# Optimization experiments

Hardware: AMD Instinct MI355X
Metric: run time of the kernel (lower is better)

Reference implementation:

```python
import jax, jax.numpy as jnp
import numpy as np
from jax import lax

B, T, I, H = 64, 784, 1, 600


def setup_inputs() -> dict:
    key = jax.random.key(0)
    ks = jax.random.split(key, 9)
    k = 1.0 / np.sqrt(H)  # pytorch LSTMCell/Linear init scale
    x = jax.random.normal(ks[0], (B, T, I), dtype=jnp.float32)
    hs0 = jax.random.normal(ks[1], (B, H), dtype=jnp.float32)
    cs0 = jax.random.normal(ks[2], (B, H), dtype=jnp.float32)
    W_ih = jax.random.normal(ks[3], (4 * H, I), dtype=jnp.float32) * k
    W_hh = jax.random.normal(ks[4], (4 * H, H), dtype=jnp.float32) * k
    b_ih = jax.random.normal(ks[5], (4 * H,), dtype=jnp.float32) * k
    b_hh = jax.random.normal(ks[6], (4 * H,), dtype=jnp.float32) * k
    W_out = jax.random.normal(ks[7], (10, H), dtype=jnp.float32) * k
    b_out = jax.random.normal(ks[8], (10,), dtype=jnp.float32) * k
    return {"x": x, "hs0": hs0, "cs0": cs0, "W_ih": W_ih, "W_hh": W_hh,
            "b_ih": b_ih, "b_hh": b_hh, "W_out": W_out, "b_out": b_out}


def reference(x, hs0, cs0, W_ih, W_hh, b_ih, b_hh, W_out, b_out):
    # Precompute input projections for all timesteps in one GEMM: [B,T,4H]
    pre = jnp.einsum('bti,gi->btg', x, W_ih) + b_ih + b_hh
    pre_t = jnp.swapaxes(pre, 0, 1)  # [T,B,4H]

    def step(carry, p):
        h, c = carry
        gates = p + h @ W_hh.T  # [B,4H], pytorch gate order i,f,g,o
        i, f, g, o = jnp.split(gates, 4, axis=-1)
        c = jax.nn.sigmoid(f) * c + jax.nn.sigmoid(i) * jnp.tanh(g)
        h = jax.nn.sigmoid(o) * jnp.tanh(c)
        return (h, c), None

    (h, _), _ = lax.scan(step, (hs0, cs0), pre_t)
    return h @ W_out.T + b_out  # [B,10]
```

## Files before the change

### kernel.cpp

```cpp
#include <hip/hip_runtime.h>
#include <math.h>

#define BB 64
#define TT 784
#define HH 600
#define CG 50
#define SGN 4
#define CPW 12
#define BW 16
#define NWG (CG*SGN)
#define BLOCK 512
#define HB4 (BW*150)
#define LDS_BYTES (84*1024)

__device__ __forceinline__ float dot4acc(float4 a, float4 b, float acc) {
    acc = fmaf(a.x, b.x, acc);
    acc = fmaf(a.y, b.y, acc);
    acc = fmaf(a.z, b.z, acc);
    acc = fmaf(a.w, b.w, acc);
    return acc;
}

__device__ __forceinline__ void ldg5_bypass(const float4* g0, const float4* g1,
                                            const float4* g2, const float4* g3,
                                            const float4* g4,
                                            float4& a, float4& b, float4& c,
                                            float4& d, float4& e) {
    asm volatile(
        "global_load_dwordx4 %0, %5, off sc0 sc1\n\t"
        "global_load_dwordx4 %1, %6, off sc0 sc1\n\t"
        "global_load_dwordx4 %2, %7, off sc0 sc1\n\t"
        "global_load_dwordx4 %3, %8, off sc0 sc1\n\t"
        "global_load_dwordx4 %4, %9, off sc0 sc1\n\t"
        "s_waitcnt vmcnt(0)"
        : "=&v"(a), "=&v"(b), "=&v"(c), "=&v"(d), "=&v"(e)
        : "v"(g0), "v"(g1), "v"(g2), "v"(g3), "v"(g4)
        : "memory");
}

__device__ __forceinline__ void stg_bypass(float* p, float v) {
    asm volatile("global_store_dword %0, %1, off sc0 sc1"
                 :: "v"(p), "v"(v) : "memory");
}

__device__ __forceinline__ float sigm_f(float v) {
    return 1.f / (1.f + __expf(-v));
}
__device__ __forceinline__ float tanh_f(float v) {
    return 1.f - 2.f / (__expf(2.f * v) + 1.f);
}

template<int MASK, int CNT>
__device__ __forceinline__ void fold(float* v, int kh) {
    const bool hi = (kh & MASK) != 0;
    #pragma unroll
    for (int i = 0; i < CNT; ++i) {
        float send = hi ? v[i] : v[i + CNT];
        float recv = __shfl_xor(send, MASK);
        v[i] = (hi ? v[i + CNT] : v[i]) + recv;
    }
}

extern "C" __global__ void __launch_bounds__(BLOCK, 2)
lstm_main(const float* __restrict__ x, const float* __restrict__ hs0,
          const float* __restrict__ cs0, const float* __restrict__ W_ih,
          const float* __restrict__ W_hh, const float* __restrict__ b_ih,
          const float* __restrict__ b_hh, float* __restrict__ hbuf,
          unsigned int* __restrict__ flags)
{
    extern __shared__ float lds[];
    float4* h4l  = (float4*)lds;
    float*  g_lds = lds + 4 * HB4;

    const int wg   = blockIdx.x;
    const int cg   = wg % CG;
    const int sg   = wg / CG;
    const int tid  = threadIdx.x;
    const int w    = tid >> 6;
    const int lane = tid & 63;
    const int bh   = lane >> 5;
    const int kh   = lane & 31;
    const int khc  = (kh < 30) ? kh : 29;
    const int b0   = sg * BW;

    float4 Wr[6][5];
    #pragma unroll
    for (int r = 0; r < 6; ++r) {
        const int row = 6 * w + r;
        const int g   = row / 12, c = row % 12;
        const float* wrow = W_hh + ((size_t)g * HH + cg * CPW + c) * HH + khc * 20;
        #pragma unroll
        for (int j = 0; j < 5; ++j)
            Wr[r][j] = (kh < 30) ? *(const float4*)(wrow + 4 * j)
                                 : make_float4(0.f, 0.f, 0.f, 0.f);
    }

    float wihv[4], biasv[4], cst = 0.f;
    const int pc = tid >> 4, pb = tid & 15;
    const int cell = cg * CPW + pc;
    const int bglob = b0 + pb;
    if (tid < 192) {
        #pragma unroll
        for (int g = 0; g < 4; ++g) {
            const int grow = g * HH + cell;
            wihv[g]  = W_ih[grow];
            biasv[g] = b_ih[grow] + b_hh[grow];
        }
        cst = cs0[(size_t)bglob * HH + cell];
    }

    const int i0 = tid, i1 = tid + 512, i2 = tid + 1024, i3 = tid + 1536;
    const int i4 = (tid + 2048 < HB4) ? tid + 2048 : HB4 - 1;

    unsigned int* myflag = &flags[wg * 16];

    for (int t = 0; t < TT; ++t) {
        float xv = 0.f;
        if (tid < 192) xv = x[(size_t)bglob * TT + t];

        if (t > 0) {
            if (tid < CG) {
                const unsigned int* f = &flags[(sg * CG + tid) * 16];
                while (__hip_atomic_load(f, __ATOMIC_RELAXED,
                                         __HIP_MEMORY_SCOPE_AGENT) < (unsigned)t)
                    __builtin_amdgcn_s_sleep(1);
            }
        }
        __syncthreads();

        {
            const float* hsrc = (t == 0) ? hs0 : (hbuf + (size_t)(t & 1) * BB * HH);
            const float4* s4 = (const float4*)hsrc + (size_t)b0 * 150;
            float4 v0, v1, v2, v3, v4;
            ldg5_bypass(s4 + i0, s4 + i1, s4 + i2, s4 + i3, s4 + i4,
                        v0, v1, v2, v3, v4);
            h4l[i0] = v0; h4l[i1] = v1; h4l[i2] = v2; h4l[i3] = v3; h4l[i4] = v4;
        }
        __syncthreads();

        float v[48] = {};
        {
            const float4* hb_base = h4l + (size_t)bh * 8 * 150 + khc * 5;
            #pragma unroll
            for (int bi = 0; bi < 8; ++bi) {
                const float4* hb = hb_base + bi * 150;
                const float4 h0 = hb[0], h1 = hb[1], h2 = hb[2],
                             h3 = hb[3], hv4 = hb[4];
                #pragma unroll
                for (int r = 0; r < 6; ++r) {
                    float a = v[r * 8 + bi];
                    a = dot4acc(Wr[r][0], h0, a);
                    a = dot4acc(Wr[r][1], h1, a);
                    a = dot4acc(Wr[r][2], h2, a);
                    a = dot4acc(Wr[r][3], h3, a);
                    a = dot4acc(Wr[r][4], hv4, a);
                    v[r * 8 + bi] = a;
                }
            }
        }

        fold<16, 24>(v, kh);
        fold<8, 12>(v, kh);
        fold<4, 6>(v, kh);
        fold<2, 3>(v, kh);
        #pragma unroll
        for (int i = 0; i < 3; ++i)
            v[i] += __shfl_xor(v[i], 1);

        if (!(kh & 1)) {
            const int vb = 3 * (kh >> 1);
            #pragma unroll
            for (int s = 0; s < 3; ++s) {
                const int val = vb + s;
                const int rowl = val >> 3, bi = val & 7;
                g_lds[(6 * w + rowl) * 16 + bh * 8 + bi] = v[s];
            }
        }
        __syncthreads();

        float* hdst = hbuf + (size_t)((t + 1) & 1) * BB * HH;
        if (tid < 192) {
            const float gi = g_lds[(0 * 12 + pc) * 16 + pb] + xv * wihv[0] + biasv[0];
            const float gf = g_lds[(1 * 12 + pc) * 16 + pb] + xv * wihv[1] + biasv[1];
            const float gg = g_lds[(2 * 12 + pc) * 16 + pb] + xv * wihv[2] + biasv[2];
            const float go = g_lds[(3 * 12 + pc) * 16 + pb] + xv * wihv[3] + biasv[3];
            const float cn = sigm_f(gf) * cst + sigm_f(gi) * tanh_f(gg);
            cst = cn;
            stg_bypass(&hdst[(size_t)bglob * HH + cell], sigm_f(go) * tanh_f(cn));
        }
        __syncthreads();
        if (tid == 0)
            __hip_atomic_store(myflag, (unsigned)(t + 1), __ATOMIC_RELAXED,
                               __HIP_MEMORY_SCOPE_AGENT);
    }
}

extern "C" __global__ void lstm_out(const float* __restrict__ hbuf0,
                                    const float* __restrict__ W_out,
                                    const float* __restrict__ b_out,
                                    float* __restrict__ out)
{
    int b = blockIdx.x;
    int lane = threadIdx.x;
    float acc[10] = {};
    for (int k = lane; k < HH; k += 64) {
        float hv = hbuf0[(size_t)b * HH + k];
        #pragma unroll
        for (int o = 0; o < 10; ++o)
            acc[o] += hv * W_out[(size_t)o * HH + k];
    }
    #pragma unroll
    for (int o = 0; o < 10; ++o) {
        float v = acc[o];
        for (int off = 32; off > 0; off >>= 1) v += __shfl_down(v, off);
        if (lane == 0) out[b * 10 + o] = v + b_out[o];
    }
}

extern "C" void kernel_launch(void* const* d_in, const int* in_sizes, int n_in,
                              void* d_out, int out_size, void* d_ws, size_t ws_size,
                              hipStream_t stream)
{
    const float* x     = (const float*)d_in[0];
    const float* hs0   = (const float*)d_in[1];
    const float* cs0   = (const float*)d_in[2];
    const float* W_ih  = (const float*)d_in[3];
    const float* W_hh  = (const float*)d_in[4];
    const float* b_ih  = (const float*)d_in[5];
    const float* b_hh  = (const float*)d_in[6];
    const float* W_out = (const float*)d_in[7];
    const float* b_out = (const float*)d_in[8];
    float* out = (float*)d_out;

    float* hbuf = (float*)d_ws;
    unsigned int* flags = (unsigned int*)((char*)d_ws + (size_t)2 * BB * HH * sizeof(float));

    hipFuncSetAttribute((const void*)lstm_main,
                        hipFuncAttributeMaxDynamicSharedMemorySize, LDS_BYTES);

    hipMemsetAsync(flags, 0, NWG * 16 * sizeof(unsigned int), stream);
    hipLaunchKernelGGL(lstm_main, dim3(NWG), dim3(BLOCK), LDS_BYTES, stream,
                       x, hs0, cs0, W_ih, W_hh, b_ih, b_hh, hbuf, flags);
    hipLaunchKernelGGL(lstm_out, dim3(BB), dim3(64), 0, stream,
                       hbuf, W_out, b_out, out);
}
```

Baseline: 4.316 ms.

## Repartition LSTM workgroups to 24 cells x 8 batches with per-producer flag waits

Changes the work split from 50 cell groups x 4 batch groups to 25 cell groups x 8 batch groups, so each lane holds 12 rows x 10 contiguous K elements of W_hh in registers. Each consumer thread now waits on its own producer workgroup's flag and copies only that producer's 24-cell slice into padded LDS. The workgroup's own freshly computed h is written straight into LDS, which shrinks the global h traffic per step and removes the serializing wait-all-then-load pattern. The cost is heavier register pressure, more flag polling per workgroup, and a new reduction and shuffle layout that could spill or add LDS bank conflicts.

```diff
diff --git a/kernel.cpp b/kernel.cpp
--- a/kernel.cpp
+++ b/kernel.cpp
@@ -4,38 +4,19 @@
 #define BB 64
 #define TT 784
 #define HH 600
-#define CG 50
-#define SGN 4
-#define CPW 12
-#define BW 16
-#define NWG (CG*SGN)
+#define KPAD 640
+#define CG 25
+#define CPW 24
+#define BWD 8
+#define NWG 200
 #define BLOCK 512
-#define HB4 (BW*150)
 #define LDS_BYTES (84*1024)
 
-__device__ __forceinline__ float dot4acc(float4 a, float4 b, float acc) {
-    acc = fmaf(a.x, b.x, acc);
-    acc = fmaf(a.y, b.y, acc);
-    acc = fmaf(a.z, b.z, acc);
-    acc = fmaf(a.w, b.w, acc);
-    return acc;
-}
-
-__device__ __forceinline__ void ldg5_bypass(const float4* g0, const float4* g1,
-                                            const float4* g2, const float4* g3,
-                                            const float4* g4,
-                                            float4& a, float4& b, float4& c,
-                                            float4& d, float4& e) {
-    asm volatile(
-        "global_load_dwordx4 %0, %5, off sc0 sc1\n\t"
-        "global_load_dwordx4 %1, %6, off sc0 sc1\n\t"
-        "global_load_dwordx4 %2, %7, off sc0 sc1\n\t"
-        "global_load_dwordx4 %3, %8, off sc0 sc1\n\t"
-        "global_load_dwordx4 %4, %9, off sc0 sc1\n\t"
-        "s_waitcnt vmcnt(0)"
-        : "=&v"(a), "=&v"(b), "=&v"(c), "=&v"(d), "=&v"(e)
-        : "v"(g0), "v"(g1), "v"(g2), "v"(g3), "v"(g4)
-        : "memory");
+__device__ __forceinline__ float sigm_f(float v) {
+    return 1.f / (1.f + __expf(-v));
+}
+__device__ __forceinline__ float tanh_f(float v) {
+    return 1.f - 2.f / (__expf(2.f * v) + 1.f);
 }
 
 __device__ __forceinline__ void stg_bypass(float* p, float v) {
@@ -43,16 +24,9 @@
                  :: "v"(p), "v"(v) : "memory");
 }
 
-__device__ __forceinline__ float sigm_f(float v) {
-    return 1.f / (1.f + __expf(-v));
-}
-__device__ __forceinline__ float tanh_f(float v) {
-    return 1.f - 2.f / (__expf(2.f * v) + 1.f);
-}
-
 template<int MASK, int CNT>
-__device__ __forceinline__ void fold(float* v, int kh) {
-    const bool hi = (kh & MASK) != 0;
+__device__ __forceinline__ void fold(float* v, int lane) {
+    const bool hi = (lane & MASK) != 0;
     #pragma unroll
     for (int i = 0; i < CNT; ++i) {
         float send = hi ? v[i] : v[i + CNT];
@@ -69,36 +43,32 @@
           unsigned int* __restrict__ flags)
 {
     extern __shared__ float lds[];
-    float4* h4l  = (float4*)lds;
-    float*  g_lds = lds + 4 * HB4;
+    float* h_lds = lds;
+    float* g_lds = lds + BWD * KPAD;
 
     const int wg   = blockIdx.x;
-    const int cg   = wg % CG;
-    const int sg   = wg / CG;
+    const int sg   = wg & 7;
+    const int cg   = wg >> 3;
     const int tid  = threadIdx.x;
     const int w    = tid >> 6;
     const int lane = tid & 63;
-    const int bh   = lane >> 5;
-    const int kh   = lane & 31;
-    const int khc  = (kh < 30) ? kh : 29;
-    const int b0   = sg * BW;
-
-    float4 Wr[6][5];
+    const int k0   = 10 * lane;
+    const int k0c  = (k0 <= HH - 10) ? k0 : (HH - 10);
+
+    float Wr[12][10];
     #pragma unroll
-    for (int r = 0; r < 6; ++r) {
-        const int row = 6 * w + r;
-        const int g   = row / 12, c = row % 12;
-        const float* wrow = W_hh + ((size_t)g * HH + cg * CPW + c) * HH + khc * 20;
-        #pragma unroll
-        for (int j = 0; j < 5; ++j)
-            Wr[r][j] = (kh < 30) ? *(const float4*)(wrow + 4 * j)
-                                 : make_float4(0.f, 0.f, 0.f, 0.f);
-    }
-
+    for (int r = 0; r < 12; ++r) {
+        const int row = 12 * w + r;
+        const int g = row / 24, c = row % 24;
+        const float* wp = W_hh + ((size_t)g * HH + CPW * cg + c) * HH + k0c;
+        #pragma unroll
+        for (int j = 0; j < 10; ++j) Wr[r][j] = wp[j];
+    }
+
+    const int pc = tid >> 3, pb = tid & 7;
+    const int cell  = CPW * cg + pc;
+    const int bglob = BWD * sg + pb;
     float wihv[4], biasv[4], cst = 0.f;
-    const int pc = tid >> 4, pb = tid & 15;
-    const int cell = cg * CPW + pc;
-    const int bglob = b0 + pb;
     if (tid < 192) {
         #pragma unroll
         for (int g = 0; g < 4; ++g) {
@@ -109,8 +79,19 @@
         cst = cs0[(size_t)bglob * HH + cell];
     }
 
-    const int i0 = tid, i1 = tid + 512, i2 = tid + 1024, i3 = tid + 1536;
-    const int i4 = (tid + 2048 < HB4) ? tid + 2048 : HB4 - 1;
+    {
+        const float4* s4 = (const float4*)(hs0 + (size_t)BWD * sg * HH);
+        for (int i = tid; i < BWD * 150; i += BLOCK) {
+            const int b = i / 150, col = i - b * 150;
+            *(float4*)&h_lds[b * KPAD + 4 * col] = s4[i];
+        }
+        if (tid < 80) {
+            const int b = tid / 10, j = tid - b * 10;
+            *(float4*)&h_lds[b * KPAD + HH + 4 * j] =
+                make_float4(0.f, 0.f, 0.f, 0.f);
+        }
+    }
+    __syncthreads();
 
     unsigned int* myflag = &flags[wg * 16];
 
@@ -119,75 +100,97 @@
         if (tid < 192) xv = x[(size_t)bglob * TT + t];
 
         if (t > 0) {
-            if (tid < CG) {
-                const unsigned int* f = &flags[(sg * CG + tid) * 16];
-                while (__hip_atomic_load(f, __ATOMIC_RELAXED,
+            if (tid < 192) {
+                const int pi  = tid >> 3;
+                const int pcg = pi + (pi >= cg);
+                const int pwg = (pcg << 3) | sg;
+                const unsigned int* fp = &flags[pwg * 16];
+                while (__hip_atomic_load(fp, __ATOMIC_RELAXED,
                                          __HIP_MEMORY_SCOPE_AGENT) < (unsigned)t)
                     __builtin_amdgcn_s_sleep(1);
+                const float4* src = (const float4*)(hbuf
+                    + (size_t)(t & 1) * BB * HH + (size_t)bglob * HH + CPW * pcg);
+                float4 r0, r1, r2, r3, r4, r5;
+                asm volatile(
+                    "global_load_dwordx4 %0, %6, off sc0 sc1\n\t"
+                    "global_load_dwordx4 %1, %6, off offset:16 sc0 sc1\n\t"
+                    "global_load_dwordx4 %2, %6, off offset:32 sc0 sc1\n\t"
+                    "global_load_dwordx4 %3, %6, off offset:48 sc0 sc1\n\t"
+                    "global_load_dwordx4 %4, %6, off offset:64 sc0 sc1\n\t"
+                    "global_load_dwordx4 %5, %6, off offset:80 sc0 sc1\n\t"
+                    "s_waitcnt vmcnt(0)"
+                    : "=&v"(r0), "=&v"(r1), "=&v"(r2),
+                      "=&v"(r3), "=&v"(r4), "=&v"(r5)
+                    : "v"(src) : "memory");
+                float4* dst = (float4*)&h_lds[pb * KPAD + CPW * pcg];
+                dst[0] = r0; dst[1] = r1; dst[2] = r2;
+                dst[3] = r3; dst[4] = r4; dst[5] = r5;
+            }
+            __syncthreads();
+        }
+
+        #pragma unroll
+        for (int bp = 0; bp < 2; ++bp) {
+            float hvf[4][10];
+            #pragma unroll
+            for (int bi = 0; bi < 4; ++bi) {
+                const float* hb = &h_lds[(4 * bp + bi) * KPAD + k0];
+                #pragma unroll
+                for (int j5 = 0; j5 < 5; ++j5) {
+                    float2 t2 = *(const float2*)(hb + 2 * j5);
+                    hvf[bi][2 * j5]     = t2.x;
+                    hvf[bi][2 * j5 + 1] = t2.y;
+                }
+            }
+            float v[48];
+            #pragma unroll
+            for (int i = 0; i < 48; ++i) v[i] = 0.f;
+            #pragma unroll
+            for (int r = 0; r < 12; ++r)
+                #pragma unroll
+                for (int j = 0; j < 10; ++j) {
+                    const float wv = Wr[r][j];
+                    v[r * 4 + 0] = fmaf(wv, hvf[0][j], v[r * 4 + 0]);
+                    v[r * 4 + 1] = fmaf(wv, hvf[1][j], v[r * 4 + 1]);
+                    v[r * 4 + 2] = fmaf(wv, hvf[2][j], v[r * 4 + 2]);
+                    v[r * 4 + 3] = fmaf(wv, hvf[3][j], v[r * 4 + 3]);
+                }
+
+            fold<1, 24>(v, lane);
+            fold<2, 12>(v, lane);
+            fold<4, 6>(v, lane);
+            fold<8, 3>(v, lane);
+            #pragma unroll
+            for (int i = 0; i < 3; ++i) {
+                v[i] += __shfl_xor(v[i], 16);
+                v[i] += __shfl_xor(v[i], 32);
+            }
+            if (lane < 16) {
+                const int idb = 3 * (((lane & 1) << 3) | (((lane >> 1) & 1) << 2)
+                                   | (((lane >> 2) & 1) << 1) | ((lane >> 3) & 1));
+                #pragma unroll
+                for (int s = 0; s < 3; ++s) {
+                    const int id = idb + s;
+                    const int r = id >> 2, bi = id & 3;
+                    g_lds[(12 * w + r) * BWD + 4 * bp + bi] = v[s];
+                }
             }
         }
         __syncthreads();
 
-        {
-            const float* hsrc = (t == 0) ? hs0 : (hbuf + (size_t)(t & 1) * BB * HH);
-            const float4* s4 = (const float4*)hsrc + (size_t)b0 * 150;
-            float4 v0, v1, v2, v3, v4;
-            ldg5_bypass(s4 + i0, s4 + i1, s4 + i2, s4 + i3, s4 + i4,
-                        v0, v1, v2, v3, v4);
-            h4l[i0] = v0; h4l[i1] = v1; h4l[i2] = v2; h4l[i3] = v3; h4l[i4] = v4;
-        }
-        __syncthreads();
-
-        float v[48] = {};
-        {
-            const float4* hb_base = h4l + (size_t)bh * 8 * 150 + khc * 5;
-            #pragma unroll
-            for (int bi = 0; bi < 8; ++bi) {
-                const float4* hb = hb_base + bi * 150;
-                const float4 h0 = hb[0], h1 = hb[1], h2 = hb[2],
-                             h3 = hb[3], hv4 = hb[4];
-                #pragma unroll
-                for (int r = 0; r < 6; ++r) {
-                    float a = v[r * 8 + bi];
-                    a = dot4acc(Wr[r][0], h0, a);
-                    a = dot4acc(Wr[r][1], h1, a);
-                    a = dot4acc(Wr[r][2], h2, a);
-                    a = dot4acc(Wr[r][3], h3, a);
-                    a = dot4acc(Wr[r][4], hv4, a);
-                    v[r * 8 + bi] = a;
-                }
-            }
-        }
-
-        fold<16, 24>(v, kh);
-        fold<8, 12>(v, kh);
-        fold<4, 6>(v, kh);
-        fold<2, 3>(v, kh);
-        #pragma unroll
-        for (int i = 0; i < 3; ++i)
-            v[i] += __shfl_xor(v[i], 1);
-
-        if (!(kh & 1)) {
-            const int vb = 3 * (kh >> 1);
-            #pragma unroll
-            for (int s = 0; s < 3; ++s) {
-                const int val = vb + s;
-                const int rowl = val >> 3, bi = val & 7;
-                g_lds[(6 * w + rowl) * 16 + bh * 8 + bi] = v[s];
-            }
-        }
-        __syncthreads();
-
-        float* hdst = hbuf + (size_t)((t + 1) & 1) * BB * HH;
         if (tid < 192) {
-            const float gi = g_lds[(0 * 12 + pc) * 16 + pb] + xv * wihv[0] + biasv[0];
-            const float gf = g_lds[(1 * 12 + pc) * 16 + pb] + xv * wihv[1] + biasv[1];
-            const float gg = g_lds[(2 * 12 + pc) * 16 + pb] + xv * wihv[2] + biasv[2];
-            const float go = g_lds[(3 * 12 + pc) * 16 + pb] + xv * wihv[3] + biasv[3];
+            const float gi = g_lds[(0 * CPW + pc) * BWD + pb] + xv * wihv[0] + biasv[0];
+            const float gf = g_lds[(1 * CPW + pc) * BWD + pb] + xv * wihv[1] + biasv[1];
+            const float gg = g_lds[(2 * CPW + pc) * BWD + pb] + xv * wihv[2] + biasv[2];
+            const float go = g_lds[(3 * CPW + pc) * BWD + pb] + xv * wihv[3] + biasv[3];
             const float cn = sigm_f(gf) * cst + sigm_f(gi) * tanh_f(gg);
             cst = cn;
-            stg_bypass(&hdst[(size_t)bglob * HH + cell], sigm_f(go) * tanh_f(cn));
-        }
+            const float hv = sigm_f(go) * tanh_f(cn);
+            h_lds[pb * KPAD + cell] = hv;
+            stg_bypass(hbuf + (size_t)((t + 1) & 1) * BB * HH
+                            + (size_t)bglob * HH + cell, hv);
+        }
+        asm volatile("s_waitcnt vmcnt(0)" ::: "memory");
         __syncthreads();
         if (tid == 0)
             __hip_atomic_store(myflag, (unsigned)(t + 1), __ATOMIC_RELAXED,
```

After: 5.320 ms. 1.23x slower.

## Per-producer flag waits with sliced h loads and packed FMA dot products

Applied to the files above, without the earlier changes.

Each block no longer waits for all 50 producer flags before copying the whole hidden state. Now 400 threads each spin on one producer's flag and load only that producer's 12-column slice for two batch rows, so loading can overlap with producers that are still running. The recurrent dot products are rewritten with 2-wide float vectors and elementwise FMA so the compiler can emit packed FMA instructions. An explicit vmcnt wait before the flag store keeps the h stores visible before the flag is published. The cost is more threads spinning on flags and a different accumulation order.

```diff
diff --git a/kernel.cpp b/kernel.cpp
--- a/kernel.cpp
+++ b/kernel.cpp
@@ -13,13 +13,7 @@
 #define HB4 (BW*150)
 #define LDS_BYTES (84*1024)
 
-__device__ __forceinline__ float dot4acc(float4 a, float4 b, float acc) {
-    acc = fmaf(a.x, b.x, acc);
-    acc = fmaf(a.y, b.y, acc);
-    acc = fmaf(a.z, b.z, acc);
-    acc = fmaf(a.w, b.w, acc);
-    return acc;
-}
+typedef float f2v __attribute__((ext_vector_type(2)));
 
 __device__ __forceinline__ void ldg5_bypass(const float4* g0, const float4* g1,
                                             const float4* g2, const float4* g3,
@@ -38,6 +32,21 @@
         : "memory");
 }
 
+__device__ __forceinline__ void ldg6_slice(const float4* base,
+                                           float4& a, float4& b, float4& c,
+                                           float4& d, float4& e, float4& f) {
+    asm volatile(
+        "global_load_dwordx4 %0, %6, off sc0 sc1\n\t"
+        "global_load_dwordx4 %1, %6, off offset:16 sc0 sc1\n\t"
+        "global_load_dwordx4 %2, %6, off offset:32 sc0 sc1\n\t"
+        "global_load_dwordx4 %3, %6, off offset:2400 sc0 sc1\n\t"
+        "global_load_dwordx4 %4, %6, off offset:2416 sc0 sc1\n\t"
+        "global_load_dwordx4 %5, %6, off offset:2432 sc0 sc1\n\t"
+        "s_waitcnt vmcnt(0)"
+        : "=&v"(a), "=&v"(b), "=&v"(c), "=&v"(d), "=&v"(e), "=&v"(f)
+        : "v"(base) : "memory");
+}
+
 __device__ __forceinline__ void stg_bypass(float* p, float v) {
     asm volatile("global_store_dword %0, %1, off sc0 sc1"
                  :: "v"(p), "v"(v) : "memory");
@@ -83,16 +92,19 @@
     const int khc  = (kh < 30) ? kh : 29;
     const int b0   = sg * BW;
 
-    float4 Wr[6][5];
+    f2v Wr2[6][10];
     #pragma unroll
     for (int r = 0; r < 6; ++r) {
         const int row = 6 * w + r;
         const int g   = row / 12, c = row % 12;
         const float* wrow = W_hh + ((size_t)g * HH + cg * CPW + c) * HH + khc * 20;
         #pragma unroll
-        for (int j = 0; j < 5; ++j)
-            Wr[r][j] = (kh < 30) ? *(const float4*)(wrow + 4 * j)
-                                 : make_float4(0.f, 0.f, 0.f, 0.f);
+        for (int j = 0; j < 5; ++j) {
+            float4 t4 = (kh < 30) ? *(const float4*)(wrow + 4 * j)
+                                  : make_float4(0.f, 0.f, 0.f, 0.f);
+            Wr2[r][2 * j]     = (f2v){t4.x, t4.y};
+            Wr2[r][2 * j + 1] = (f2v){t4.z, t4.w};
+        }
     }
 
     float wihv[4], biasv[4], cst = 0.f;
@@ -112,51 +124,70 @@
     const int i0 = tid, i1 = tid + 512, i2 = tid + 1024, i3 = tid + 1536;
     const int i4 = (tid + 2048 < HB4) ? tid + 2048 : HB4 - 1;
 
+    const int sp    = tid >> 3;
+    const int bsl   = tid & 7;
+    const unsigned int* pflag = &flags[(sg * CG + sp) * 16];
+    const int pdst  = (2 * bsl) * 150 + 3 * sp;
+
     unsigned int* myflag = &flags[wg * 16];
 
     for (int t = 0; t < TT; ++t) {
         float xv = 0.f;
         if (tid < 192) xv = x[(size_t)bglob * TT + t];
 
-        if (t > 0) {
-            if (tid < CG) {
-                const unsigned int* f = &flags[(sg * CG + tid) * 16];
-                while (__hip_atomic_load(f, __ATOMIC_RELAXED,
-                                         __HIP_MEMORY_SCOPE_AGENT) < (unsigned)t)
-                    __builtin_amdgcn_s_sleep(1);
-            }
-        }
-        __syncthreads();
-
-        {
-            const float* hsrc = (t == 0) ? hs0 : (hbuf + (size_t)(t & 1) * BB * HH);
-            const float4* s4 = (const float4*)hsrc + (size_t)b0 * 150;
+        if (t == 0) {
+            const float4* s4 = (const float4*)hs0 + (size_t)b0 * 150;
             float4 v0, v1, v2, v3, v4;
             ldg5_bypass(s4 + i0, s4 + i1, s4 + i2, s4 + i3, s4 + i4,
                         v0, v1, v2, v3, v4);
             h4l[i0] = v0; h4l[i1] = v1; h4l[i2] = v2; h4l[i3] = v3; h4l[i4] = v4;
+        } else if (tid < 400) {
+            while (__hip_atomic_load(pflag, __ATOMIC_RELAXED,
+                                     __HIP_MEMORY_SCOPE_AGENT) < (unsigned)t)
+                __builtin_amdgcn_s_sleep(1);
+            const float4* src = (const float4*)(hbuf + (size_t)(t & 1) * BB * HH
+                + (size_t)(b0 + 2 * bsl) * HH + CPW * sp);
+            float4 r0, r1, r2, r3, r4, r5;
+            ldg6_slice(src, r0, r1, r2, r3, r4, r5);
+            h4l[pdst]       = r0; h4l[pdst + 1]       = r1; h4l[pdst + 2]       = r2;
+            h4l[pdst + 150] = r3; h4l[pdst + 150 + 1] = r4; h4l[pdst + 150 + 2] = r5;
         }
         __syncthreads();
 
-        float v[48] = {};
+        float v[48];
         {
+            f2v acc2[6][8];
+            #pragma unroll
+            for (int r = 0; r < 6; ++r)
+                #pragma unroll
+                for (int bi = 0; bi < 8; ++bi)
+                    acc2[r][bi] = (f2v){0.f, 0.f};
+
             const float4* hb_base = h4l + (size_t)bh * 8 * 150 + khc * 5;
             #pragma unroll
             for (int bi = 0; bi < 8; ++bi) {
                 const float4* hb = hb_base + bi * 150;
-                const float4 h0 = hb[0], h1 = hb[1], h2 = hb[2],
-                             h3 = hb[3], hv4 = hb[4];
+                const float4 A = hb[0], B = hb[1], C = hb[2],
+                             D = hb[3], E = hb[4];
+                f2v h2[10];
+                h2[0] = (f2v){A.x, A.y}; h2[1] = (f2v){A.z, A.w};
+                h2[2] = (f2v){B.x, B.y}; h2[3] = (f2v){B.z, B.w};
+                h2[4] = (f2v){C.x, C.y}; h2[5] = (f2v){C.z, C.w};
+                h2[6] = (f2v){D.x, D.y}; h2[7] = (f2v){D.z, D.w};
+                h2[8] = (f2v){E.x, E.y}; h2[9] = (f2v){E.z, E.w};
                 #pragma unroll
-                for (int r = 0; r < 6; ++r) {
-                    float a = v[r * 8 + bi];
-                    a = dot4acc(Wr[r][0], h0, a);
-                    a = dot4acc(Wr[r][1], h1, a);
-                    a = dot4acc(Wr[r][2], h2, a);
-                    a = dot4acc(Wr[r][3], h3, a);
-                    a = dot4acc(Wr[r][4], hv4, a);
-                    v[r * 8 + bi] = a;
-                }
+                for (int r = 0; r < 6; ++r)
+                    #pragma unroll
+                    for (int j = 0; j < 10; ++j)
+                        acc2[r][bi] = __builtin_elementwise_fma(Wr2[r][j],
+                                                                h2[j],
+                                                                acc2[r][bi]);
             }
+            #pragma unroll
+            for (int r = 0; r < 6; ++r)
+                #pragma unroll
+                for (int bi = 0; bi < 8; ++bi)
+                    v[r * 8 + bi] = acc2[r][bi][0] + acc2[r][bi][1];
         }
 
         fold<16, 24>(v, kh);
@@ -188,6 +219,7 @@
             cst = cn;
             stg_bypass(&hdst[(size_t)bglob * HH + cell], sigm_f(go) * tanh_f(cn));
         }
+        asm volatile("s_waitcnt vmcnt(0)" ::: "memory");
         __syncthreads();
         if (tid == 0)
             __hip_atomic_store(myflag, (unsigned)(t + 1), __ATOMIC_RELAXED,
```

New measurement: 5.119 ms. 1.19x slower.
